# Kernel optimization log

Measured on AMD Instinct MI355X. Metric: run time of the kernel, lower is better.

## Reference

```python
import jax, jax.numpy as jnp
import numpy as np

HEADS = 8
AGENT = 49
POOL = 7   # sqrt(AGENT)
WIN = 32


def _adaptive_avg_pool(x, out):
    # x: (b, h, w, c) -> (b, out, out, c), replicating torch AdaptiveAvgPool2d bins
    h = x.shape[1]
    starts = [(i * h) // out for i in range(out)]
    ends = [-((-(i + 1) * h) // out) for i in range(out)]
    rows = jnp.stack([x[:, s:e].mean(axis=1) for s, e in zip(starts, ends)], axis=1)      # (b,out,w,c)
    return jnp.stack([rows[:, :, s:e].mean(axis=2) for s, e in zip(starts, ends)], axis=2)  # (b,out,out,c)


def setup_inputs() -> dict:
    key = jax.random.key(0)
    ks = jax.random.split(key, 13)
    b, n, c = 32, WIN * WIN, 256
    std = 0.02
    return {
        "x": jax.random.normal(ks[0], (b, n + 1, c), jnp.float32),
        "qkv_w": jax.random.normal(ks[1], (3 * c, c), jnp.float32) * std,
        "proj_w": jax.random.normal(ks[2], (c, c), jnp.float32) * std,
        "proj_b": jnp.zeros((c,), jnp.float32),
        "dwc_w": jax.random.normal(ks[3], (c, 1, 3, 3), jnp.float32) * std,  # torch (C_out, 1, kh, kw)
        "dwc_b": jnp.zeros((c,), jnp.float32),
        "an_bias": jax.random.normal(ks[4], (HEADS, AGENT, 7, 7), jnp.float32) * std,
        "ah_bias": jax.random.normal(ks[5], (1, HEADS, AGENT, WIN, 1), jnp.float32) * std,
        "aw_bias": jax.random.normal(ks[6], (1, HEADS, AGENT, 1, WIN), jnp.float32) * std,
        "na_bias": jax.random.normal(ks[7], (HEADS, AGENT, 7, 7), jnp.float32) * std,
        "ha_bias": jax.random.normal(ks[8], (1, HEADS, WIN, 1, AGENT), jnp.float32) * std,
        "wa_bias": jax.random.normal(ks[9], (1, HEADS, 1, WIN, AGENT), jnp.float32) * std,
    }


def reference(x, qkv_w, proj_w, proj_b, dwc_w, dwc_b,
              an_bias, ah_bias, aw_bias, na_bias, ha_bias, wa_bias):
    cls_tok, xs = x[:, :1], x[:, 1:]
    b, n, c = xs.shape
    h = w = WIN
    hd = c // HEADS
    scale = hd ** -0.5

    qkv = xs @ qkv_w.T                                   # (b, n, 3c)
    q, k, v = jnp.split(qkv, 3, axis=-1)                 # each (b, n, c)

    # agent tokens: adaptive avg pool of q over the spatial grid
    agents = _adaptive_avg_pool(q.reshape(b, h, w, c), POOL).reshape(b, AGENT, c)

    qh = q.reshape(b, n, HEADS, hd).transpose(0, 2, 1, 3)        # (b,H,n,d)
    kh = k.reshape(b, n, HEADS, hd).transpose(0, 2, 1, 3)
    vh = v.reshape(b, n, HEADS, hd).transpose(0, 2, 1, 3)
    ah = agents.reshape(b, AGENT, HEADS, hd).transpose(0, 2, 1, 3)  # (b,H,A,d)

    # stage 1: agent <-> k/v, bias interpolated 7x7 -> WINxWIN (half-pixel bilinear == torch align_corners=False)
    pb1 = jax.image.resize(an_bias, (HEADS, AGENT, WIN, WIN), method='bilinear').reshape(1, HEADS, AGENT, n)
    pb2 = (ah_bias + aw_bias).reshape(1, HEADS, AGENT, n)
    agent_attn = jax.nn.softmax((ah * scale) @ kh.transpose(0, 1, 3, 2) + pb1 + pb2, axis=-1)  # (b,H,A,n)
    agent_v = agent_attn @ vh                                    # (b,H,A,d)

    # stage 2: q <-> agents
    ab1 = jax.image.resize(na_bias, (HEADS, AGENT, WIN, WIN), method='bilinear').reshape(1, HEADS, AGENT, n).transpose(0, 1, 3, 2)
    ab2 = (ha_bias + wa_bias).reshape(1, HEADS, n, AGENT)
    q_attn = jax.nn.softmax((qh * scale) @ ah.transpose(0, 1, 3, 2) + ab1 + ab2, axis=-1)      # (b,H,n,A)
    out = (q_attn @ agent_v).transpose(0, 2, 1, 3).reshape(b, n, c)

    # depthwise conv residual on v (NHWC)
    v_img = vh.transpose(0, 2, 1, 3).reshape(b, h, w, c)
    kern = dwc_w.transpose(2, 3, 1, 0)                            # (3,3,1,c) HWIO
    dwc = jax.lax.conv_general_dilated(v_img, kern, (1, 1), 'SAME',
                                       feature_group_count=c,
                                       dimension_numbers=('NHWC', 'HWIO', 'NHWC')) + dwc_b
    out = out + dwc.reshape(b, n, c)

    out = jnp.concatenate([cls_tok, out], axis=1)
    return out @ proj_w.T + proj_b
```

## Files before the change

### kernel.cpp

```cpp
#include <hip/hip_runtime.h>
#include <hip/hip_bf16.h>

#define BATCH 32
#define NTOK 1024
#define CH 256
#define HEADS 8
#define HD 32
#define AGENTS 49
#define WIN 32
#define QKV_N 768
#define SCALE 0.17677669529663687f

typedef unsigned short u16;
typedef __attribute__((ext_vector_type(2))) unsigned short u16x2;
typedef __attribute__((ext_vector_type(8))) unsigned short u16x8;
typedef __attribute__((ext_vector_type(8))) short short8;
typedef __attribute__((ext_vector_type(4))) float f32x4;

__device__ __forceinline__ void gload_lds16(const void* g, const void* l) {
    __builtin_amdgcn_global_load_lds(
        (const __attribute__((address_space(1))) unsigned int*)g,
        (__attribute__((address_space(3))) unsigned int*)l, 16, 0, 0);
}

__device__ __forceinline__ u16 f2bf1(float f) {
    unsigned u = __builtin_bit_cast(unsigned, f);
    u += 0x7fffu + ((u >> 16) & 1u);
    return (u16)(u >> 16);
}
__device__ __forceinline__ float bf2f(u16 v) {
    unsigned u = ((unsigned)v) << 16;
    return __builtin_bit_cast(float, u);
}

__global__ void f2bf_kernel(const float* __restrict__ in, u16* __restrict__ out, int n8) {
    int i = blockIdx.x * 256 + threadIdx.x;
    if (i >= n8) return;
    float4 v0 = ((const float4*)in)[i * 2];
    float4 v1 = ((const float4*)in)[i * 2 + 1];
    u16x8 o;
    o[0] = f2bf1(v0.x); o[1] = f2bf1(v0.y); o[2] = f2bf1(v0.z); o[3] = f2bf1(v0.w);
    o[4] = f2bf1(v1.x); o[5] = f2bf1(v1.y); o[6] = f2bf1(v1.z); o[7] = f2bf1(v1.w);
    ((u16x8*)out)[i] = o;
}

__global__ __launch_bounds__(256) void gemm_bf16(const u16* __restrict__ A,
                                                 const u16* __restrict__ B,
                                                 float* __restrict__ C,
                                                 u16* __restrict__ C16,
                                                 int M, int N, int K,
                                                 const float* __restrict__ bias,
                                                 int amode) {
    __shared__ u16 As[128 * 32];
    __shared__ u16 Bs[128 * 32];
    const int tid = threadIdx.x;
    const int lane = tid & 63;
    const int wid = tid >> 6;
    const int row0 = blockIdx.x * 128, col0 = blockIdx.y * 128;
    const int wr = wid >> 1, wc = wid & 1;
    const int fr = lane & 15, fq = lane >> 4;

    f32x4 acc[4][4];
#pragma unroll
    for (int m = 0; m < 4; ++m)
#pragma unroll
        for (int n = 0; n < 4; ++n) acc[m][n] = (f32x4)(0.f);

    for (int k0 = 0; k0 < K; k0 += 32) {
#pragma unroll
        for (int r = 0; r < 2; ++r) {
            int trow = (tid >> 2) + r * 64;
            int tcol = (tid & 3) * 8;
            size_t aoff;
            int grow = row0 + trow;
            if (amode == 1) {
                int bb = grow >> 10, nn = grow & 1023;
                aoff = ((size_t)(bb * 1025 + nn + 1)) * 256 + (size_t)(k0 + tcol);
            } else {
                if (grow >= M) grow = M - 1;
                aoff = (size_t)grow * K + (size_t)(k0 + tcol);
            }
            gload_lds16(A + aoff, (const char*)As + wid * 1024 + r * 4096);
            int brow = col0 + trow;
            gload_lds16(B + (size_t)brow * K + (size_t)(k0 + tcol),
                        (const char*)Bs + wid * 1024 + r * 4096);
        }
        __syncthreads();

        short8 af[4], bf[4];
#pragma unroll
        for (int m = 0; m < 4; ++m)
            af[m] = *(const short8*)&As[(wr * 64 + m * 16 + fr) * 32 + fq * 8];
#pragma unroll
        for (int n = 0; n < 4; ++n)
            bf[n] = *(const short8*)&Bs[(wc * 64 + n * 16 + fr) * 32 + fq * 8];
#pragma unroll
        for (int m = 0; m < 4; ++m)
#pragma unroll
            for (int n = 0; n < 4; ++n)
                acc[m][n] = __builtin_amdgcn_mfma_f32_16x16x32_bf16(af[m], bf[n], acc[m][n], 0, 0, 0);
        __syncthreads();
    }

#pragma unroll
    for (int m = 0; m < 4; ++m) {
#pragma unroll
        for (int j = 0; j < 4; ++j) {
            int row = row0 + wr * 64 + m * 16 + fq * 4 + j;
            if (row < M) {
#pragma unroll
                for (int n = 0; n < 4; ++n) {
                    int col = col0 + wc * 64 + n * 16 + fr;
                    float v = acc[m][n][j];
                    if (bias) v += bias[col];
                    if (C16) C16[(size_t)row * N + col] = f2bf1(v);
                    else     C[(size_t)row * N + col] = v;
                }
            }
        }
    }
}

__global__ __launch_bounds__(256) void pool_kernel(const u16* __restrict__ qkvb,
                                                   float* __restrict__ agents) {
    int b = blockIdx.x / 7, py = blockIdx.x % 7;
    int ch = threadIdx.x;
    int ys = py * 32 / 7, ye = ((py + 1) * 32 + 6) / 7;
    float acc[7];
#pragma unroll
    for (int i = 0; i < 7; ++i) acc[i] = 0.f;
    for (int y = ys; y < ye; ++y) {
        const u16* rowp = qkvb + ((size_t)(b * NTOK + y * 32)) * QKV_N + ch;
#pragma unroll
        for (int PX = 0; PX < 7; ++PX) {
            const int xs = PX * 32 / 7, xe = ((PX + 1) * 32 + 6) / 7;
            float s = 0.f;
            for (int x = xs; x < xe; ++x) s += bf2f(rowp[(size_t)x * QKV_N]);
            acc[PX] += s;
        }
    }
    int rcnt = ye - ys;
#pragma unroll
    for (int PX = 0; PX < 7; ++PX) {
        const int xs = PX * 32 / 7, xe = ((PX + 1) * 32 + 6) / 7;
        agents[((size_t)(b * AGENTS + py * 7 + PX)) * CH + ch] =
            acc[PX] / (float)(rcnt * (xe - xs));
    }
}

__device__ inline float bilin7(const float* __restrict__ m, float sy, float sx) {
    float fy0 = floorf(sy), fx0 = floorf(sx);
    int y0 = (int)fy0, x0 = (int)fx0;
    float fy = sy - fy0, fx = sx - fx0;
    int y0c = min(max(y0, 0), 6), y1c = min(max(y0 + 1, 0), 6);
    int x0c = min(max(x0, 0), 6), x1c = min(max(x0 + 1, 0), 6);
    float v00 = m[y0c * 7 + x0c], v01 = m[y0c * 7 + x1c];
    float v10 = m[y1c * 7 + x0c], v11 = m[y1c * 7 + x1c];
    return (1.f - fy) * ((1.f - fx) * v00 + fx * v01) + fy * ((1.f - fx) * v10 + fx * v11);
}

__global__ void pb_kernel(const float* __restrict__ an, const float* __restrict__ ahb,
                          const float* __restrict__ awb, float* __restrict__ pbn) {
    int h = blockIdx.x >> 6, a = blockIdx.x & 63;
    if (a >= AGENTS) {
        for (int n = threadIdx.x; n < NTOK; n += 256)
            pbn[((size_t)(h * NTOK + n)) * 64 + a] = 0.f;
        return;
    }
    const float* m = an + (h * AGENTS + a) * 49;
    for (int n = threadIdx.x; n < NTOK; n += 256) {
        int y = n >> 5, x = n & 31;
        float v = bilin7(m, (y + 0.5f) * (7.f / 32.f) - 0.5f, (x + 0.5f) * (7.f / 32.f) - 0.5f);
        v += ahb[(h * AGENTS + a) * 32 + y] + awb[(h * AGENTS + a) * 32 + x];
        pbn[((size_t)(h * NTOK + n)) * 64 + a] = v;
    }
}

__global__ void ab_kernel(const float* __restrict__ na, const float* __restrict__ hab,
                          const float* __restrict__ wab, float* __restrict__ abT) {
    int idx = blockIdx.x * 256 + threadIdx.x;
    if (idx >= HEADS * AGENTS * NTOK) return;
    int h = idx / (AGENTS * NTOK);
    int r = idx % (AGENTS * NTOK);
    int a = r / NTOK, n = r % NTOK;
    int y = n >> 5, x = n & 31;
    const float* m = na + (h * AGENTS + a) * 49;
    float v = bilin7(m, (y + 0.5f) * (7.f / 32.f) - 0.5f, (x + 0.5f) * (7.f / 32.f) - 0.5f);
    v += hab[(h * 32 + y) * AGENTS + a] + wab[(h * 32 + x) * AGENTS + a];
    abT[idx] = v;
}

#define VTP 1038
__global__ __launch_bounds__(512) void fused_attn(const u16* __restrict__ qkvb,
                                                  const float* __restrict__ agents,
                                                  const float* __restrict__ pbn,
                                                  const float* __restrict__ abT,
                                                  const float* __restrict__ dwc_w,
                                                  const float* __restrict__ dwc_b,
                                                  u16* __restrict__ outbf) {
    int b = blockIdx.x >> 3, h = blockIdx.x & 7;
    int tid = threadIdx.x, lane = tid & 63, w = tid >> 6;
    const int fr = lane & 15, fq = lane >> 4;

    __shared__ u16 ah_lds[64 * 32];
    __shared__ u16 Vt[32 * VTP];
    __shared__ float PO[8][2304];
    __shared__ float lsum_lds[8][64];
    __shared__ u16 avT[32][72];
    __shared__ float w9[9][32];
    __shared__ float bia[32];

    u16*   Pw = (u16*)&PO[w][0];
    float* Ow = &PO[w][0];

    for (int li = tid; li < 64 * 32; li += 512) {
        int a = li >> 5, d = li & 31;
        float v = (a < AGENTS) ? agents[((size_t)(b * AGENTS + a)) * CH + h * HD + d] * SCALE : 0.f;
        ah_lds[li] = f2bf1(v);
    }
    for (int li = tid; li < 512 * 4; li += 512) {
        int p = li >> 2, d8 = (li & 3) * 8;
        const u16* g0 = &qkvb[((size_t)(b * NTOK + 2 * p)) * QKV_N + 2 * CH + h * HD + d8];
        u16x8 va = *(const u16x8*)g0;
        u16x8 vb = *(const u16x8*)(g0 + QKV_N);
#pragma unroll
        for (int j = 0; j < 8; ++j) {
            u16x2 w2; w2[0] = va[j]; w2[1] = vb[j];
            *(u16x2*)&Vt[(d8 + j) * VTP + 2 * p] = w2;
        }
    }
    for (int li = tid; li < 288; li += 512) {
        int t = li >> 5, d = li & 31;
        w9[t][d] = dwc_w[(h * HD + d) * 9 + t];
    }
    if (tid < 32) bia[tid] = dwc_b[h * HD + tid];
    __syncthreads();

    short8 ahf[4];
#pragma unroll
    for (int mt = 0; mt < 4; ++mt)
        ahf[mt] = *(const short8*)&ah_lds[(mt * 16 + fr) * 32 + fq * 8];

    short8 kf[2][4];
#pragma unroll
    for (int c2 = 0; c2 < 2; ++c2)
#pragma unroll
        for (int nt = 0; nt < 4; ++nt)
            kf[c2][nt] = *(const short8*)&qkvb[((size_t)(b * NTOK + w * 128 + c2 * 64 + nt * 16 + fr)) * QKV_N + CH + h * HD + fq * 8];

    float lsum[4][4];
#pragma unroll
    for (int mt = 0; mt < 4; ++mt)
#pragma unroll
        for (int j = 0; j < 4; ++j) lsum[mt][j] = 0.f;
    f32x4 accA[4][2];
#pragma unroll
    for (int mt = 0; mt < 4; ++mt)
#pragma unroll
        for (int ntd = 0; ntd < 2; ++ntd) accA[mt][ntd] = (f32x4)(0.f);

    const float* pbnh = pbn + (size_t)h * NTOK * 64;

#pragma unroll
    for (int c2 = 0; c2 < 2; ++c2) {
        int tb = w * 128 + c2 * 64;

        f32x4 pbq[2][4];
#pragma unroll
        for (int nt = 0; nt < 4; ++nt)
            pbq[0][nt] = *(const f32x4*)&pbnh[(size_t)(tb + nt * 16 + fr) * 64 + fq * 4];

#pragma unroll
        for (int mt = 0; mt < 4; ++mt) {
            f32x4 accS[4];
#pragma unroll
            for (int nt = 0; nt < 4; ++nt)
                accS[nt] = __builtin_amdgcn_mfma_f32_16x16x32_bf16(ahf[mt], kf[c2][nt], (f32x4)(0.f), 0, 0, 0);
            if (mt < 3) {
#pragma unroll
                for (int nt = 0; nt < 4; ++nt)
                    pbq[(mt + 1) & 1][nt] = *(const f32x4*)&pbnh[(size_t)(tb + nt * 16 + fr) * 64 + (mt + 1) * 16 + fq * 4];
            }
#pragma unroll
            for (int j = 0; j < 4; ++j) {
                int a = mt * 16 + fq * 4 + j;
#pragma unroll
                for (int nt = 0; nt < 4; ++nt) {
                    float e = __expf(accS[nt][j] + pbq[mt & 1][nt][j]);
                    lsum[mt][j] += e;
                    Pw[a * 72 + nt * 16 + fr] = f2bf1(e);
                }
            }
        }

        short8 pf[4][2], vf[2][2];
#pragma unroll
        for (int mt = 0; mt < 4; ++mt)
#pragma unroll
            for (int kc = 0; kc < 2; ++kc)
                pf[mt][kc] = *(const short8*)&Pw[(mt * 16 + fr) * 72 + kc * 32 + fq * 8];
#pragma unroll
        for (int ntd = 0; ntd < 2; ++ntd)
#pragma unroll
            for (int kc = 0; kc < 2; ++kc)
                vf[ntd][kc] = *(const short8*)&Vt[(ntd * 16 + fr) * VTP + tb + kc * 32 + fq * 8];

#pragma unroll
        for (int mt = 0; mt < 4; ++mt)
#pragma unroll
            for (int kc = 0; kc < 2; ++kc)
#pragma unroll
                for (int ntd = 0; ntd < 2; ++ntd)
                    accA[mt][ntd] = __builtin_amdgcn_mfma_f32_16x16x32_bf16(pf[mt][kc], vf[ntd][kc], accA[mt][ntd], 0, 0, 0);
    }

#pragma unroll
    for (int mt = 0; mt < 4; ++mt)
#pragma unroll
        for (int j = 0; j < 4; ++j) {
            float s = lsum[mt][j];
            s += __shfl_xor(s, 1);
            s += __shfl_xor(s, 2);
            s += __shfl_xor(s, 4);
            s += __shfl_xor(s, 8);
            lsum[mt][j] = s;
        }
    if (fr == 0) {
#pragma unroll
        for (int mt = 0; mt < 4; ++mt)
#pragma unroll
            for (int j = 0; j < 4; ++j)
                lsum_lds[w][mt * 16 + fq * 4 + j] = lsum[mt][j];
    }

    asm volatile("s_waitcnt lgkmcnt(0)" ::: "memory");
    __builtin_amdgcn_sched_barrier(0);

#pragma unroll
    for (int mt = 0; mt < 4; ++mt)
#pragma unroll
        for (int ntd = 0; ntd < 2; ++ntd)
#pragma unroll
            for (int j = 0; j < 4; ++j)
                Ow[(mt * 16 + fq * 4 + j) * 32 + ntd * 16 + fr] = accA[mt][ntd][j];

    __syncthreads();

    for (int li = tid; li < 64 * HD; li += 512) {
        int a = li & 63, d = li >> 6;
        float val = 0.f;
        if (a < AGENTS) {
            float L = 0.f, o = 0.f;
#pragma unroll
            for (int ww = 0; ww < 8; ++ww) {
                o += PO[ww][a * 32 + d];
                L += lsum_lds[ww][a];
            }
            val = o / L;
        }
        avT[d][a] = f2bf1(val);
    }
    __syncthreads();

    short8 avf[2][2];
#pragma unroll
    for (int ntd = 0; ntd < 2; ++ntd)
#pragma unroll
        for (int kc = 0; kc < 2; ++kc)
            avf[ntd][kc] = *(const short8*)&avT[ntd * 16 + fr][kc * 32 + fq * 8];

    short8 qf2[4][2];
#pragma unroll
    for (int hh = 0; hh < 4; ++hh)
#pragma unroll
        for (int mt2 = 0; mt2 < 2; ++mt2)
            qf2[hh][mt2] = *(const short8*)(qkvb + ((size_t)(b * NTOK + w * 128 + hh * 32 + mt2 * 16 + fr)) * QKV_N + h * HD + fq * 8);

    const float* abTh = abT + (size_t)h * AGENTS * NTOK;

#pragma unroll
    for (int hh = 0; hh < 4; ++hh) {
        int hb = w * 128 + hh * 32;

        f32x4 abv[2][4];
#pragma unroll
        for (int mt2 = 0; mt2 < 2; ++mt2)
#pragma unroll
            for (int nt = 0; nt < 4; ++nt)
                abv[mt2][nt] = *(const f32x4*)&abTh[(size_t)min(nt * 16 + fr, AGENTS - 1) * NTOK + hb + mt2 * 16 + fq * 4];

#pragma unroll
        for (int mt2 = 0; mt2 < 2; ++mt2) {
            f32x4 accS[4];
#pragma unroll
            for (int nt = 0; nt < 4; ++nt)
                accS[nt] = __builtin_amdgcn_mfma_f32_16x16x32_bf16(qf2[hh][mt2], ahf[nt], (f32x4)(0.f), 0, 0, 0);

            float e[4][4];
            float ps[4];
#pragma unroll
            for (int j = 0; j < 4; ++j) ps[j] = 0.f;
#pragma unroll
            for (int j = 0; j < 4; ++j) {
#pragma unroll
                for (int nt = 0; nt < 4; ++nt) {
                    int a = nt * 16 + fr;
                    float s = accS[nt][j] + abv[mt2][nt][j];
                    float ev = (a < AGENTS) ? __expf(s) : 0.f;
                    e[j][nt] = ev;
                    ps[j] += ev;
                }
            }
#pragma unroll
            for (int j = 0; j < 4; ++j) {
                ps[j] += __shfl_xor(ps[j], 1);
                ps[j] += __shfl_xor(ps[j], 2);
                ps[j] += __shfl_xor(ps[j], 4);
                ps[j] += __shfl_xor(ps[j], 8);
            }
#pragma unroll
            for (int j = 0; j < 4; ++j) {
                float inv = 1.f / ps[j];
                int tl = mt2 * 16 + fq * 4 + j;
#pragma unroll
                for (int nt = 0; nt < 4; ++nt)
                    Pw[tl * 68 + nt * 16 + fr] = f2bf1(e[j][nt] * inv);
            }
        }

        short8 pf2[2][2];
#pragma unroll
        for (int mt2 = 0; mt2 < 2; ++mt2)
#pragma unroll
            for (int kc = 0; kc < 2; ++kc)
                pf2[mt2][kc] = *(const short8*)&Pw[(mt2 * 16 + fr) * 68 + kc * 32 + fq * 8];

        f32x4 accO[2][2];
#pragma unroll
        for (int mt2 = 0; mt2 < 2; ++mt2)
#pragma unroll
            for (int ntd = 0; ntd < 2; ++ntd) accO[mt2][ntd] = (f32x4)(0.f);
#pragma unroll
        for (int mt2 = 0; mt2 < 2; ++mt2)
#pragma unroll
            for (int kc = 0; kc < 2; ++kc)
#pragma unroll
                for (int ntd = 0; ntd < 2; ++ntd)
                    accO[mt2][ntd] = __builtin_amdgcn_mfma_f32_16x16x32_bf16(pf2[mt2][kc], avf[ntd][kc], accO[mt2][ntd], 0, 0, 0);

        int y = w * 4 + hh;
#pragma unroll
        for (int ntd = 0; ntd < 2; ++ntd) {
            int d = ntd * 16 + fr;
            float wv[9];
#pragma unroll
            for (int t = 0; t < 9; ++t) wv[t] = w9[t][d];
            float bv = bia[d];
            const u16* Vd = &Vt[d * VTP];
#pragma unroll
            for (int mt2 = 0; mt2 < 2; ++mt2) {
                int x0 = mt2 * 16 + fq * 4;
                float sp[3][8];
#pragma unroll
                for (int dy = 0; dy < 3; ++dy) {
                    int yy = y - 1 + dy;
                    if (yy >= 0 && yy < 32) {
                        int base = yy * 32 + x0 - 2;
                        u16x2 r0 = *(const u16x2*)&Vd[base];
                        u16x2 r1 = *(const u16x2*)&Vd[base + 2];
                        u16x2 r2 = *(const u16x2*)&Vd[base + 4];
                        u16x2 r3 = *(const u16x2*)&Vd[base + 6];
                        sp[dy][0] = bf2f(r0[0]); sp[dy][1] = bf2f(r0[1]);
                        sp[dy][2] = bf2f(r1[0]); sp[dy][3] = bf2f(r1[1]);
                        sp[dy][4] = bf2f(r2[0]); sp[dy][5] = bf2f(r2[1]);
                        sp[dy][6] = bf2f(r3[0]); sp[dy][7] = bf2f(r3[1]);
                    } else {
#pragma unroll
                        for (int k = 0; k < 8; ++k) sp[dy][k] = 0.f;
                    }
                }
                float vv[3][6];
#pragma unroll
                for (int dy = 0; dy < 3; ++dy)
#pragma unroll
                    for (int k = 0; k < 6; ++k) {
                        int xx = x0 - 1 + k;
                        vv[dy][k] = (xx >= 0 && xx < 32) ? sp[dy][k + 1] : 0.f;
                    }
#pragma unroll
                for (int j = 0; j < 4; ++j) {
                    float o = accO[mt2][ntd][j] + bv;
#pragma unroll
                    for (int dy = 0; dy < 3; ++dy)
#pragma unroll
                        for (int dx = 0; dx < 3; ++dx)
                            o = fmaf(wv[dy * 3 + dx], vv[dy][j + dx], o);
                    int n = y * 32 + x0 + j;
                    outbf[((size_t)(b * 1025 + 1 + n)) * CH + h * HD + d] = f2bf1(o);
                }
            }
        }
    }
}
#undef VTP

extern "C" void kernel_launch(void* const* d_in, const int* in_sizes, int n_in,
                              void* d_out, int out_size, void* d_ws, size_t ws_size,
                              hipStream_t stream) {
    const float* x      = (const float*)d_in[0];
    const float* qkv_w  = (const float*)d_in[1];
    const float* proj_w = (const float*)d_in[2];
    const float* proj_b = (const float*)d_in[3];
    const float* dwc_w  = (const float*)d_in[4];
    const float* dwc_b  = (const float*)d_in[5];
    const float* an_b   = (const float*)d_in[6];
    const float* ah_b   = (const float*)d_in[7];
    const float* aw_b   = (const float*)d_in[8];
    const float* na_b   = (const float*)d_in[9];
    const float* ha_b   = (const float*)d_in[10];
    const float* wa_b   = (const float*)d_in[11];
    float* out = (float*)d_out;

    float* ws      = (float*)d_ws;
    u16*   qkvb    = (u16*)ws;
    float* agents  = ws + 12582912;
    float* pbn     = agents + 401408;
    float* abT     = pbn + 524288;
    u16* xbf  = (u16*)(abT + 401408);
    u16* qwbf = xbf + 8396800;
    u16* pwbf = qwbf + 196608;

    f2bf_kernel<<<4100, 256, 0, stream>>>(x, xbf, 8396800 / 8);
    f2bf_kernel<<<96, 256, 0, stream>>>(qkv_w, qwbf, 196608 / 8);
    f2bf_kernel<<<32, 256, 0, stream>>>(proj_w, pwbf, 65536 / 8);
    gemm_bf16<<<dim3(256, 6), 256, 0, stream>>>(xbf, qwbf, nullptr, qkvb, 32768, 768, 256, nullptr, 1);
    pool_kernel<<<BATCH * 7, 256, 0, stream>>>(qkvb, agents);
    pb_kernel<<<HEADS * 64, 256, 0, stream>>>(an_b, ah_b, aw_b, pbn);
    ab_kernel<<<(HEADS * AGENTS * NTOK + 255) / 256, 256, 0, stream>>>(na_b, ha_b, wa_b, abT);
    fused_attn<<<BATCH * HEADS, 512, 0, stream>>>(qkvb, agents, pbn, abT, dwc_w, dwc_b, xbf);
    gemm_bf16<<<dim3(257, 2), 256, 0, stream>>>(xbf, pwbf, out, nullptr, 32800, 256, 256, proj_b, 0);
}
```

Measured before the change: 133.8 us.

## Write V transposed from QKV GEMM and fuse agent pooling into attention

The QKV GEMM epilogue now writes the V columns into a per-(batch, channel) transposed bf16 buffer, so the attention kernel can copy V^T into LDS with contiguous vector loads instead of transposing it on the fly. The separate pooling kernel is removed and each attention block computes its own agent tokens directly from q. LDS strides are padded (VTP 1040, O stride 33) and the reduction loop is reindexed to reduce bank conflicts. The cost is scattered 2-byte transposed stores in the GEMM epilogue and redundant pooling reads of q inside the attention kernel.

```diff
diff --git a/kernel.cpp b/kernel.cpp
--- a/kernel.cpp
+++ b/kernel.cpp
@@ -48,6 +48,7 @@
                                                  const u16* __restrict__ B,
                                                  float* __restrict__ C,
                                                  u16* __restrict__ C16,
+                                                 u16* __restrict__ vT,
                                                  int M, int N, int K,
                                                  const float* __restrict__ bias,
                                                  int amode) {
@@ -113,38 +114,16 @@
                     int col = col0 + wc * 64 + n * 16 + fr;
                     float v = acc[m][n][j];
                     if (bias) v += bias[col];
-                    if (C16) C16[(size_t)row * N + col] = f2bf1(v);
-                    else     C[(size_t)row * N + col] = v;
+                    if (vT && col >= 512) {
+                        vT[((size_t)((row >> 10) * 256 + (col - 512))) * 1024 + (row & 1023)] = f2bf1(v);
+                    } else if (C16) {
+                        C16[(size_t)row * N + col] = f2bf1(v);
+                    } else {
+                        C[(size_t)row * N + col] = v;
+                    }
                 }
             }
         }
-    }
-}
-
-__global__ __launch_bounds__(256) void pool_kernel(const u16* __restrict__ qkvb,
-                                                   float* __restrict__ agents) {
-    int b = blockIdx.x / 7, py = blockIdx.x % 7;
-    int ch = threadIdx.x;
-    int ys = py * 32 / 7, ye = ((py + 1) * 32 + 6) / 7;
-    float acc[7];
-#pragma unroll
-    for (int i = 0; i < 7; ++i) acc[i] = 0.f;
-    for (int y = ys; y < ye; ++y) {
-        const u16* rowp = qkvb + ((size_t)(b * NTOK + y * 32)) * QKV_N + ch;
-#pragma unroll
-        for (int PX = 0; PX < 7; ++PX) {
-            const int xs = PX * 32 / 7, xe = ((PX + 1) * 32 + 6) / 7;
-            float s = 0.f;
-            for (int x = xs; x < xe; ++x) s += bf2f(rowp[(size_t)x * QKV_N]);
-            acc[PX] += s;
-        }
-    }
-    int rcnt = ye - ys;
-#pragma unroll
-    for (int PX = 0; PX < 7; ++PX) {
-        const int xs = PX * 32 / 7, xe = ((PX + 1) * 32 + 6) / 7;
-        agents[((size_t)(b * AGENTS + py * 7 + PX)) * CH + ch] =
-            acc[PX] / (float)(rcnt * (xe - xs));
     }
 }
 
@@ -190,9 +169,10 @@
     abT[idx] = v;
 }
 
-#define VTP 1038
+#define VTP 1040
+#define OSTR 33
 __global__ __launch_bounds__(512) void fused_attn(const u16* __restrict__ qkvb,
-                                                  const float* __restrict__ agents,
+                                                  const u16* __restrict__ vt_g,
                                                   const float* __restrict__ pbn,
                                                   const float* __restrict__ abT,
                                                   const float* __restrict__ dwc_w,
@@ -215,18 +195,24 @@
 
     for (int li = tid; li < 64 * 32; li += 512) {
         int a = li >> 5, d = li & 31;
-        float v = (a < AGENTS) ? agents[((size_t)(b * AGENTS + a)) * CH + h * HD + d] * SCALE : 0.f;
-        ah_lds[li] = f2bf1(v);
-    }
-    for (int li = tid; li < 512 * 4; li += 512) {
-        int p = li >> 2, d8 = (li & 3) * 8;
-        const u16* g0 = &qkvb[((size_t)(b * NTOK + 2 * p)) * QKV_N + 2 * CH + h * HD + d8];
-        u16x8 va = *(const u16x8*)g0;
-        u16x8 vb = *(const u16x8*)(g0 + QKV_N);
-#pragma unroll
-        for (int j = 0; j < 8; ++j) {
-            u16x2 w2; w2[0] = va[j]; w2[1] = vb[j];
-            *(u16x2*)&Vt[(d8 + j) * VTP + 2 * p] = w2;
+        float val = 0.f;
+        if (a < AGENTS) {
+            int py = a / 7, px = a % 7;
+            int ys = py * 32 / 7, ye = ((py + 1) * 32 + 6) / 7;
+            int xs = px * 32 / 7, xe = ((px + 1) * 32 + 6) / 7;
+            float s = 0.f;
+            for (int y = ys; y < ye; ++y)
+                for (int x = xs; x < xe; ++x)
+                    s += bf2f(qkvb[((size_t)(b * NTOK + y * 32 + x)) * QKV_N + h * HD + d]);
+            val = s / (float)((ye - ys) * (xe - xs)) * SCALE;
+        }
+        ah_lds[li] = f2bf1(val);
+    }
+    {
+        const u16* src = vt_g + ((size_t)(b * 256 + h * HD)) * 1024;
+        for (int li = tid; li < 32 * 128; li += 512) {
+            int r = li >> 7, c = li & 127;
+            *(u16x8*)&Vt[r * VTP + c * 8] = *(const u16x8*)&src[r * 1024 + c * 8];
         }
     }
     for (int li = tid; li < 288; li += 512) {
@@ -342,18 +328,18 @@
         for (int ntd = 0; ntd < 2; ++ntd)
 #pragma unroll
             for (int j = 0; j < 4; ++j)
-                Ow[(mt * 16 + fq * 4 + j) * 32 + ntd * 16 + fr] = accA[mt][ntd][j];
+                Ow[(mt * 16 + fq * 4 + j) * OSTR + ntd * 16 + fr] = accA[mt][ntd][j];
 
     __syncthreads();
 
     for (int li = tid; li < 64 * HD; li += 512) {
-        int a = li & 63, d = li >> 6;
+        int d = li & 31, a = li >> 5;
         float val = 0.f;
         if (a < AGENTS) {
             float L = 0.f, o = 0.f;
 #pragma unroll
             for (int ww = 0; ww < 8; ++ww) {
-                o += PO[ww][a * 32 + d];
+                o += PO[ww][a * OSTR + d];
                 L += lsum_lds[ww][a];
             }
             val = o / L;
@@ -503,6 +489,7 @@
     }
 }
 #undef VTP
+#undef OSTR
 
 extern "C" void kernel_launch(void* const* d_in, const int* in_sizes, int n_in,
                               void* d_out, int out_size, void* d_ws, size_t ws_size,
@@ -523,20 +510,19 @@
 
     float* ws      = (float*)d_ws;
     u16*   qkvb    = (u16*)ws;
-    float* agents  = ws + 12582912;
-    float* pbn     = agents + 401408;
+    float* pbn     = ws + 12582912;
     float* abT     = pbn + 524288;
-    u16* xbf  = (u16*)(abT + 401408);
+    u16*   vtg     = (u16*)(abT + 401408);
+    u16* xbf  = vtg + 8388608;
     u16* qwbf = xbf + 8396800;
     u16* pwbf = qwbf + 196608;
 
     f2bf_kernel<<<4100, 256, 0, stream>>>(x, xbf, 8396800 / 8);
     f2bf_kernel<<<96, 256, 0, stream>>>(qkv_w, qwbf, 196608 / 8);
     f2bf_kernel<<<32, 256, 0, stream>>>(proj_w, pwbf, 65536 / 8);
-    gemm_bf16<<<dim3(256, 6), 256, 0, stream>>>(xbf, qwbf, nullptr, qkvb, 32768, 768, 256, nullptr, 1);
-    pool_kernel<<<BATCH * 7, 256, 0, stream>>>(qkvb, agents);
+    gemm_bf16<<<dim3(256, 6), 256, 0, stream>>>(xbf, qwbf, nullptr, qkvb, vtg, 32768, 768, 256, nullptr, 1);
     pb_kernel<<<HEADS * 64, 256, 0, stream>>>(an_b, ah_b, aw_b, pbn);
     ab_kernel<<<(HEADS * AGENTS * NTOK + 255) / 256, 256, 0, stream>>>(na_b, ha_b, wa_b, abT);
-    fused_attn<<<BATCH * HEADS, 512, 0, stream>>>(qkvb, agents, pbn, abT, dwc_w, dwc_b, xbf);
-    gemm_bf16<<<dim3(257, 2), 256, 0, stream>>>(xbf, pwbf, out, nullptr, 32800, 256, 256, proj_b, 0);
-}
+    fused_attn<<<BATCH * HEADS, 512, 0, stream>>>(qkvb, vtg, pbn, abT, dwc_w, dwc_b, xbf);
+    gemm_bf16<<<dim3(257, 2), 256, 0, stream>>>(xbf, pwbf, out, nullptr, nullptr, 32800, 256, 256, proj_b, 0);
+}
```

New measurement: 161.9 us. 1.21x slower.
